# Performance work log

Measured on AMD Instinct MI355X. Metric: run time of the kernel, lower is better.

## Reference

```python
import math
import jax, jax.numpy as jnp
import numpy as np

DIM = 128
M = 256  # num_projections
DEQUANT_SCALE = math.sqrt(math.pi / 2) / M


def setup_inputs() -> dict:
    key = jax.random.key(0)
    k1, k2, k3 = jax.random.split(key, 3)
    query = jax.random.normal(k1, (4, 32768, DIM), dtype=jnp.float32)
    kv = jax.random.normal(k2, (4, 32768, DIM), dtype=jnp.float32)
    S = jax.random.normal(k3, (M, DIM), dtype=jnp.float32)
    return {"query": query, "key": kv, "S": S}


def reference(query, key, S):
    # quantize: sign bits of JL projection of keys  -> (..., M) in {-1, 0, +1}
    quantized_key = jnp.sign(jnp.einsum('bnd,md->bnm', key, S))
    # asymmetric estimator: full-precision projected query x sign-bit key
    query_projected = jnp.einsum('bnd,md->bnm', query, S)
    est = DEQUANT_SCALE * jnp.sum(query_projected * quantized_key, axis=-1)
    return est  # (4, 32768)
```

## Files before the change

kernel.cpp:

```cpp
#include <hip/hip_runtime.h>
#include <stdint.h>


typedef __attribute__((ext_vector_type(8))) short bf16x8;
typedef __attribute__((ext_vector_type(4))) float f32x4;

#define DEQUANT 0.004895758348888673f
#define DELTA 0.01f
#define SEG 512

static __device__ __forceinline__ unsigned short f2bf(float f) {
  union { float f; uint32_t u; } v; v.f = f;
  return (unsigned short)((v.u + 0x7FFFu + ((v.u >> 16) & 1u)) >> 16);
}
static __device__ __forceinline__ float bf2f(unsigned short h) {
  union { uint32_t u; float f; } v; v.u = ((uint32_t)h) << 16;
  return v.f;
}

__global__ void qjl_prep(const float* __restrict__ S, unsigned short* __restrict__ ST) {
  int i = blockIdx.x * blockDim.x + threadIdx.x;
  const int j = i & 7;
  const int l = (i >> 3) & 63;
  const int c = (i >> 9) & 3;
  const int t = (i >> 11) & 3;
  const int h = (i >> 13) & 1;
  const int s = i >> 14;
  const int m = s * 64 + t * 16 + (l & 15);
  const int k = c * 32 + (l >> 4) * 8 + j;
  const float f = S[m * 128 + k];
  const unsigned short hi = f2bf(f);
  ST[i] = h ? f2bf(f - bf2f(hi)) : hi;
}

__global__ __launch_bounds__(256, 2) void qjl_main(
    const float* __restrict__ Q, const float* __restrict__ K,
    const unsigned short* __restrict__ ST,
    float* __restrict__ out, unsigned int* __restrict__ blockCount,
    unsigned int* __restrict__ wl) {
  __shared__ unsigned int l_cnt;
  __shared__ unsigned int l_ent[SEG];

  const int wave = threadIdx.x >> 6;
  const int lane = threadIdx.x & 63;
  const int col  = lane & 15;
  const int kg   = lane >> 4;
  const int rowbase = (blockIdx.x * 4 + wave) * 32;

  if (threadIdx.x == 0) l_cnt = 0u;
  __syncthreads();

  bf16x8 qB[2][4], khB[2][4], klB[2][4];
#pragma unroll
  for (int a = 0; a < 2; ++a) {
    const float* qrow = Q + (size_t)(rowbase + a * 16 + col) * 128 + kg * 8;
    const float* krow = K + (size_t)(rowbase + a * 16 + col) * 128 + kg * 8;
#pragma unroll
    for (int c = 0; c < 4; ++c) {
      float qf[8], kf[8];
      *(float4*)(&qf[0]) = *(const float4*)(qrow + c * 32);
      *(float4*)(&qf[4]) = *(const float4*)(qrow + c * 32 + 4);
      *(float4*)(&kf[0]) = *(const float4*)(krow + c * 32);
      *(float4*)(&kf[4]) = *(const float4*)(krow + c * 32 + 4);
#pragma unroll
      for (int j = 0; j < 8; ++j) {
        qB[a][c][j] = (short)f2bf(qf[j]);
        unsigned short h = f2bf(kf[j]);
        khB[a][c][j] = (short)h;
        klB[a][c][j] = (short)f2bf(kf[j] - bf2f(h));
      }
    }
  }

  float part[2] = {0.f, 0.f};

#pragma unroll
  for (int s = 0; s < 4; ++s) {
    f32x4 accq[2][4], acck[2][4];
#pragma unroll
    for (int a = 0; a < 2; ++a)
#pragma unroll
      for (int t = 0; t < 4; ++t) {
        accq[a][t] = (f32x4){0.f, 0.f, 0.f, 0.f};
        acck[a][t] = (f32x4){0.f, 0.f, 0.f, 0.f};
      }
#pragma unroll
    for (int t = 0; t < 4; ++t) {
#pragma unroll
      for (int c = 0; c < 4; ++c) {
        const bf16x8 bh = *(const bf16x8*)(ST + (size_t)(((s * 2 + 0) * 4 + t) * 4 + c) * 512 + lane * 8);
        const bf16x8 bl = *(const bf16x8*)(ST + (size_t)(((s * 2 + 1) * 4 + t) * 4 + c) * 512 + lane * 8);
#pragma unroll
        for (int a = 0; a < 2; ++a) {
          accq[a][t] = __builtin_amdgcn_mfma_f32_16x16x32_bf16(bh, qB[a][c],  accq[a][t], 0, 0, 0);
          acck[a][t] = __builtin_amdgcn_mfma_f32_16x16x32_bf16(bh, khB[a][c], acck[a][t], 0, 0, 0);
          acck[a][t] = __builtin_amdgcn_mfma_f32_16x16x32_bf16(bh, klB[a][c], acck[a][t], 0, 0, 0);
          acck[a][t] = __builtin_amdgcn_mfma_f32_16x16x32_bf16(bl, khB[a][c], acck[a][t], 0, 0, 0);
        }
      }
    }
#pragma unroll
    for (int a = 0; a < 2; ++a)
#pragma unroll
      for (int t = 0; t < 4; ++t)
#pragma unroll
        for (int r = 0; r < 4; ++r) {
          const float kp = acck[a][t][r];
          const float sg = (kp > 0.f) ? 1.f : ((kp < 0.f) ? -1.f : 0.f);
          part[a] += sg * accq[a][t][r];
          if (__builtin_fabsf(kp) < DELTA) {
            const int m = s * 64 + t * 16 + kg * 4 + r;
            const int row = rowbase + a * 16 + col;
            const unsigned int code = (kp > 0.f) ? 1u : ((kp < 0.f) ? 2u : 0u);
            const unsigned int idx = atomicAdd(&l_cnt, 1u);
            if (idx < SEG) l_ent[idx] = (code << 25) | ((unsigned int)row << 8) | (unsigned int)m;
          }
        }
  }

#pragma unroll
  for (int a = 0; a < 2; ++a) {
    float v = part[a];
    v += __shfl_xor(v, 16);
    v += __shfl_xor(v, 32);
    if (lane < 16) out[rowbase + a * 16 + lane] = v * DEQUANT;
  }

  __syncthreads();
  unsigned int n = l_cnt;
  if (n > SEG) n = SEG;
  if (threadIdx.x == 0) blockCount[blockIdx.x] = n;
  for (unsigned int i = threadIdx.x; i < n; i += 256)
    wl[(size_t)blockIdx.x * SEG + i] = l_ent[i];
}

__global__ __launch_bounds__(256) void qjl_fix(
    const float* __restrict__ Q, const float* __restrict__ K, const float* __restrict__ S,
    float* __restrict__ out, const unsigned int* __restrict__ blockCount,
    const unsigned int* __restrict__ wl) {
  const unsigned int n = blockCount[blockIdx.x];
  const int lane = threadIdx.x & 63;
  const int wave = threadIdx.x >> 6;
  for (unsigned int e = wave; e < n; e += 4) {
    const unsigned int ent = wl[(size_t)blockIdx.x * SEG + e];
    const unsigned int m = ent & 255u;
    const unsigned int row = (ent >> 8) & 0x1FFFFu;
    const unsigned int code = ent >> 25;
    const float s_old = (code == 1u) ? 1.f : ((code == 2u) ? -1.f : 0.f);
    const float* kr = K + (size_t)row * 128;
    const float* qr = Q + (size_t)row * 128;
    const float* sr = S + (size_t)m * 128;
    const int d = lane * 2;
    double kp = (double)kr[d] * (double)sr[d] + (double)kr[d + 1] * (double)sr[d + 1];
    double qp = (double)qr[d] * (double)sr[d] + (double)qr[d + 1] * (double)sr[d + 1];
#pragma unroll
    for (int mask = 1; mask < 64; mask <<= 1) {
      kp += __shfl_xor(kp, mask);
      qp += __shfl_xor(qp, mask);
    }
    if (lane == 0) {
      const float s_new = (kp > 0.0) ? 1.f : ((kp < 0.0) ? -1.f : 0.f);
      const float dlt = (s_new - s_old) * (float)qp * DEQUANT;
      if (dlt != 0.f) atomicAdd(out + row, dlt);
    }
  }
}

extern "C" void kernel_launch(void* const* d_in, const int* in_sizes, int n_in,
                              void* d_out, int out_size, void* d_ws, size_t ws_size,
                              hipStream_t stream) {
  const float* Q = (const float*)d_in[0];
  const float* K = (const float*)d_in[1];
  const float* S = (const float*)d_in[2];
  float* out = (float*)d_out;
  const int rows = in_sizes[0] / 128;
  const int sn = in_sizes[2];
  const int nblk = rows / 128;

  unsigned short* ST = (unsigned short*)d_ws;
  unsigned int* blockCount = (unsigned int*)((char*)d_ws + (size_t)sn * 4);
  unsigned int* wl = blockCount + nblk;

  hipLaunchKernelGGL(qjl_prep, dim3((2 * sn) / 256), dim3(256), 0, stream, S, ST);
  hipLaunchKernelGGL(qjl_main, dim3(nblk), dim3(256), 0, stream,
                     Q, K, ST, out, blockCount, wl);
  hipLaunchKernelGGL(qjl_fix, dim3(nblk), dim3(256), 0, stream,
                     Q, K, S, out, blockCount, wl);
}
```

Baseline: 219.2 us.

## Split key and query passes via sign bitmasks to cut registers, raise occupancy

```diff
diff --git a/kernel.cpp b/kernel.cpp
--- a/kernel.cpp
+++ b/kernel.cpp
@@ -33,7 +33,7 @@
   ST[i] = h ? f2bf(f - bf2f(hi)) : hi;
 }
 
-__global__ __launch_bounds__(256, 2) void qjl_main(
+__global__ __launch_bounds__(256, 3) void qjl_main(
     const float* __restrict__ Q, const float* __restrict__ K,
     const unsigned short* __restrict__ ST,
     float* __restrict__ out, unsigned int* __restrict__ blockCount,
@@ -50,72 +50,110 @@
   if (threadIdx.x == 0) l_cnt = 0u;
   __syncthreads();
 
-  bf16x8 qB[2][4], khB[2][4], klB[2][4];
-#pragma unroll
-  for (int a = 0; a < 2; ++a) {
-    const float* qrow = Q + (size_t)(rowbase + a * 16 + col) * 128 + kg * 8;
-    const float* krow = K + (size_t)(rowbase + a * 16 + col) * 128 + kg * 8;
-#pragma unroll
-    for (int c = 0; c < 4; ++c) {
-      float qf[8], kf[8];
-      *(float4*)(&qf[0]) = *(const float4*)(qrow + c * 32);
-      *(float4*)(&qf[4]) = *(const float4*)(qrow + c * 32 + 4);
-      *(float4*)(&kf[0]) = *(const float4*)(krow + c * 32);
-      *(float4*)(&kf[4]) = *(const float4*)(krow + c * 32 + 4);
-#pragma unroll
-      for (int j = 0; j < 8; ++j) {
-        qB[a][c][j] = (short)f2bf(qf[j]);
-        unsigned short h = f2bf(kf[j]);
-        khB[a][c][j] = (short)h;
-        klB[a][c][j] = (short)f2bf(kf[j] - bf2f(h));
-      }
-    }
-  }
-
-  float part[2] = {0.f, 0.f};
-
-#pragma unroll
-  for (int s = 0; s < 4; ++s) {
-    f32x4 accq[2][4], acck[2][4];
-#pragma unroll
-    for (int a = 0; a < 2; ++a)
+  unsigned int smask[2][2] = {{0u, 0u}, {0u, 0u}};
+
+  {
+    bf16x8 khB[2][4], klB[2][4];
+#pragma unroll
+    for (int a = 0; a < 2; ++a) {
+      const float* krow = K + (size_t)(rowbase + a * 16 + col) * 128 + kg * 8;
+#pragma unroll
+      for (int c = 0; c < 4; ++c) {
+        float kf[8];
+        *(float4*)(&kf[0]) = *(const float4*)(krow + c * 32);
+        *(float4*)(&kf[4]) = *(const float4*)(krow + c * 32 + 4);
+#pragma unroll
+        for (int j = 0; j < 8; ++j) {
+          unsigned short h = f2bf(kf[j]);
+          khB[a][c][j] = (short)h;
+          klB[a][c][j] = (short)f2bf(kf[j] - bf2f(h));
+        }
+      }
+    }
+
+#pragma unroll
+    for (int s = 0; s < 4; ++s) {
+      f32x4 acck[2][4];
+#pragma unroll
+      for (int a = 0; a < 2; ++a)
+#pragma unroll
+        for (int t = 0; t < 4; ++t) acck[a][t] = (f32x4){0.f, 0.f, 0.f, 0.f};
 #pragma unroll
       for (int t = 0; t < 4; ++t) {
-        accq[a][t] = (f32x4){0.f, 0.f, 0.f, 0.f};
-        acck[a][t] = (f32x4){0.f, 0.f, 0.f, 0.f};
-      }
-#pragma unroll
-    for (int t = 0; t < 4; ++t) {
-#pragma unroll
-      for (int c = 0; c < 4; ++c) {
-        const bf16x8 bh = *(const bf16x8*)(ST + (size_t)(((s * 2 + 0) * 4 + t) * 4 + c) * 512 + lane * 8);
-        const bf16x8 bl = *(const bf16x8*)(ST + (size_t)(((s * 2 + 1) * 4 + t) * 4 + c) * 512 + lane * 8);
-#pragma unroll
-        for (int a = 0; a < 2; ++a) {
-          accq[a][t] = __builtin_amdgcn_mfma_f32_16x16x32_bf16(bh, qB[a][c],  accq[a][t], 0, 0, 0);
-          acck[a][t] = __builtin_amdgcn_mfma_f32_16x16x32_bf16(bh, khB[a][c], acck[a][t], 0, 0, 0);
-          acck[a][t] = __builtin_amdgcn_mfma_f32_16x16x32_bf16(bh, klB[a][c], acck[a][t], 0, 0, 0);
-          acck[a][t] = __builtin_amdgcn_mfma_f32_16x16x32_bf16(bl, khB[a][c], acck[a][t], 0, 0, 0);
-        }
-      }
-    }
-#pragma unroll
-    for (int a = 0; a < 2; ++a)
-#pragma unroll
-      for (int t = 0; t < 4; ++t)
-#pragma unroll
-        for (int r = 0; r < 4; ++r) {
-          const float kp = acck[a][t][r];
-          const float sg = (kp > 0.f) ? 1.f : ((kp < 0.f) ? -1.f : 0.f);
-          part[a] += sg * accq[a][t][r];
-          if (__builtin_fabsf(kp) < DELTA) {
-            const int m = s * 64 + t * 16 + kg * 4 + r;
-            const int row = rowbase + a * 16 + col;
-            const unsigned int code = (kp > 0.f) ? 1u : ((kp < 0.f) ? 2u : 0u);
-            const unsigned int idx = atomicAdd(&l_cnt, 1u);
-            if (idx < SEG) l_ent[idx] = (code << 25) | ((unsigned int)row << 8) | (unsigned int)m;
+#pragma unroll
+        for (int c = 0; c < 4; ++c) {
+          const bf16x8 bh = *(const bf16x8*)(ST + (size_t)(((s * 2 + 0) * 4 + t) * 4 + c) * 512 + lane * 8);
+          const bf16x8 bl = *(const bf16x8*)(ST + (size_t)(((s * 2 + 1) * 4 + t) * 4 + c) * 512 + lane * 8);
+#pragma unroll
+          for (int a = 0; a < 2; ++a) {
+            acck[a][t] = __builtin_amdgcn_mfma_f32_16x16x32_bf16(bh, khB[a][c], acck[a][t], 0, 0, 0);
+            acck[a][t] = __builtin_amdgcn_mfma_f32_16x16x32_bf16(bh, klB[a][c], acck[a][t], 0, 0, 0);
+            acck[a][t] = __builtin_amdgcn_mfma_f32_16x16x32_bf16(bl, khB[a][c], acck[a][t], 0, 0, 0);
           }
         }
+      }
+#pragma unroll
+      for (int a = 0; a < 2; ++a)
+#pragma unroll
+        for (int t = 0; t < 4; ++t)
+#pragma unroll
+          for (int r = 0; r < 4; ++r) {
+            const float kp = acck[a][t][r];
+            if (kp > 0.f) smask[a][s >> 1] |= (1u << ((s & 1) * 16 + t * 4 + r));
+            if (__builtin_fabsf(kp) < DELTA) {
+              const int m = s * 64 + t * 16 + kg * 4 + r;
+              const int row = rowbase + a * 16 + col;
+              const unsigned int code = (kp > 0.f) ? 1u : 2u;
+              const unsigned int idx = atomicAdd(&l_cnt, 1u);
+              if (idx < SEG) l_ent[idx] = (code << 25) | ((unsigned int)row << 8) | (unsigned int)m;
+            }
+          }
+    }
+  }
+
+  float part[2] = {0.f, 0.f};
+  {
+    bf16x8 qB[2][4];
+#pragma unroll
+    for (int a = 0; a < 2; ++a) {
+      const float* qrow = Q + (size_t)(rowbase + a * 16 + col) * 128 + kg * 8;
+#pragma unroll
+      for (int c = 0; c < 4; ++c) {
+        float qf[8];
+        *(float4*)(&qf[0]) = *(const float4*)(qrow + c * 32);
+        *(float4*)(&qf[4]) = *(const float4*)(qrow + c * 32 + 4);
+#pragma unroll
+        for (int j = 0; j < 8; ++j) qB[a][c][j] = (short)f2bf(qf[j]);
+      }
+    }
+
+#pragma unroll
+    for (int s = 0; s < 4; ++s) {
+      f32x4 accq[2][4];
+#pragma unroll
+      for (int a = 0; a < 2; ++a)
+#pragma unroll
+        for (int t = 0; t < 4; ++t) accq[a][t] = (f32x4){0.f, 0.f, 0.f, 0.f};
+#pragma unroll
+      for (int t = 0; t < 4; ++t) {
+#pragma unroll
+        for (int c = 0; c < 4; ++c) {
+          const bf16x8 bh = *(const bf16x8*)(ST + (size_t)(((s * 2 + 0) * 4 + t) * 4 + c) * 512 + lane * 8);
+#pragma unroll
+          for (int a = 0; a < 2; ++a)
+            accq[a][t] = __builtin_amdgcn_mfma_f32_16x16x32_bf16(bh, qB[a][c], accq[a][t], 0, 0, 0);
+        }
+      }
+#pragma unroll
+      for (int a = 0; a < 2; ++a)
+#pragma unroll
+        for (int t = 0; t < 4; ++t)
+#pragma unroll
+          for (int r = 0; r < 4; ++r) {
+            const unsigned int bit = (smask[a][s >> 1] >> ((s & 1) * 16 + t * 4 + r)) & 1u;
+            part[a] += bit ? accq[a][t][r] : -accq[a][t][r];
+          }
+    }
   }
 
 #pragma unroll
@@ -146,7 +184,7 @@
     const unsigned int m = ent & 255u;
     const unsigned int row = (ent >> 8) & 0x1FFFFu;
     const unsigned int code = ent >> 25;
-    const float s_old = (code == 1u) ? 1.f : ((code == 2u) ? -1.f : 0.f);
+    const float s_old = (code == 1u) ? 1.f : -1.f;
     const float* kr = K + (size_t)row * 128;
     const float* qr = Q + (size_t)row * 128;
     const float* sr = S + (size_t)m * 128;
```

Result: slower. 224.3 us (+2.3%).
